# Performance work log

Measured on AMD Instinct MI355X. Metric: run time of the kernel, lower is better.

## Reference

```python
import jax, jax.numpy as jnp
import numpy as np

N_NODES = 50000
N_EDGES = 640000
IN_CH = 32
OUT_CH = 64
H1 = 2 * IN_CH   # 64
H2 = 4 * IN_CH   # 128


def _sage_conv(x, src, dst, w_l, b_l, w_r, n_nodes):
    """PyG SAGEConv (mean aggr): out = mean_{j in N(i)} x_j @ w_l + b_l + x_i @ w_r."""
    msg = x[src]                                                  # [E, d] gather
    agg = jax.ops.segment_sum(msg, dst, num_segments=n_nodes)    # [N, d]
    cnt = jax.ops.segment_sum(jnp.ones_like(dst, x.dtype), dst, num_segments=n_nodes)
    mean = agg / jnp.maximum(cnt, 1.0)[:, None]                   # empty neighborhoods -> 0
    return mean @ w_l + b_l + x @ w_r


def setup_inputs() -> dict:
    key = jax.random.key(0)
    ks = jax.random.split(key, 9)
    x = jax.random.normal(ks[0], (N_NODES, IN_CH), dtype=jnp.float32)
    edge_index = jax.random.randint(ks[1], (2, N_EDGES), 0, N_NODES, dtype=jnp.int32)

    def glorot(k, shape):
        fan_in, fan_out = shape
        s = jnp.sqrt(6.0 / (fan_in + fan_out))
        return jax.random.uniform(k, shape, jnp.float32, -s, s)

    return {
        "x": x,
        "edge_index": edge_index,
        "w1_l": glorot(ks[2], (IN_CH, H1)), "b1": jnp.zeros((H1,), jnp.float32),
        "w1_r": glorot(ks[3], (IN_CH, H1)),
        "w2_l": glorot(ks[4], (H1, H2)), "b2": jnp.zeros((H2,), jnp.float32),
        "w2_r": glorot(ks[5], (H1, H2)),
        "w3_l": glorot(ks[6], (H2, OUT_CH)), "b3": jnp.zeros((OUT_CH,), jnp.float32),
        "w3_r": glorot(ks[7], (H2, OUT_CH)),
    }


def reference(x, edge_index, w1_l, b1, w1_r, w2_l, b2, w2_r, w3_l, b3, w3_r):
    n = x.shape[0]
    src, dst = edge_index[0], edge_index[1]
    h = jax.nn.relu(_sage_conv(x, src, dst, w1_l, b1, w1_r, n))
    h = jax.nn.relu(_sage_conv(h, src, dst, w2_l, b2, w2_r, n))
    return _sage_conv(h, src, dst, w3_l, b3, w3_r, n)
```

## Files before the change

### kernel.cpp

```cpp
#include <hip/hip_runtime.h>


typedef short bf8 __attribute__((ext_vector_type(8)));
typedef short bf4 __attribute__((ext_vector_type(4)));
typedef float f32x4 __attribute__((ext_vector_type(4)));

__device__ inline ushort bf16rn(float f) {
    unsigned u = __float_as_uint(f);
    return (ushort)((u + 0x7FFFu + ((u >> 16) & 1u)) >> 16);
}
__device__ inline float bf16tof(ushort h) {
    return __uint_as_float(((unsigned)h) << 16);
}
__device__ inline void split8(const float4 pa, const float4 pb, bf8& hi, bf8& lo) {
    const float v[8] = {pa.x, pa.y, pa.z, pa.w, pb.x, pb.y, pb.z, pb.w};
#pragma unroll
    for (int j = 0; j < 8; ++j) {
        const ushort h = bf16rn(v[j]);
        hi[j] = (short)h;
        lo[j] = (short)bf16rn(v[j] - bf16tof(h));
    }
}

__global__ __launch_bounds__(256) void prep_kernel(
    const float* __restrict__ x,
    const float* __restrict__ w1l, const float* __restrict__ w1r,
    const float* __restrict__ w2l, const float* __restrict__ w2r,
    const float* __restrict__ w3l, const float* __restrict__ w3r,
    ushort* __restrict__ wprep, int* __restrict__ cnt,
    ushort* __restrict__ xh, int nN, int nCntZero)
{
    const int g = blockIdx.x * 256 + threadIdx.x;
    const int n = gridDim.x * 256;
    for (int f = g; f < 9216; f += n) {
        int base, KCs, oc0, d0, wstride;
        const float *wa, *wb;
        if (f < 1024)      { base = 0;    KCs = 2; oc0 = 0;  wa = w1l; wb = w1r; d0 = 32;  wstride = 64;  }
        else if (f < 3072) { base = 1024; KCs = 4; oc0 = 0;  wa = w2l; wb = w2r; d0 = 64;  wstride = 128; }
        else if (f < 5120) { base = 3072; KCs = 4; oc0 = 64; wa = w2l; wb = w2r; d0 = 64;  wstride = 128; }
        else if (f < 7168) { base = 5120; KCs = 4; oc0 = 0;  wa = w3l; wb = w3l; d0 = 128; wstride = 64;  }
        else               { base = 7168; KCs = 4; oc0 = 0;  wa = w3r; wb = w3r; d0 = 128; wstride = 64;  }
        const int local = f - base;
        const int lane = local & 63;
        const int s = (local >> 6) & 1;
        const int kcct = local >> 7;
        const int kc = kcct % KCs;
        const int ct = kcct / KCs;
        const int col = oc0 + ct * 16 + (lane & 15);
        const int k0 = kc * 32 + (lane >> 4) * 8;
        ushort h8[8];
#pragma unroll
        for (int j = 0; j < 8; ++j) {
            const int k = k0 + j;
            const float* wr = (k < d0) ? (wa + (size_t)k * wstride)
                                       : (wb + (size_t)(k - d0) * wstride);
            const float v = wr[col];
            const ushort h = bf16rn(v);
            h8[j] = (s == 0) ? h : bf16rn(v - bf16tof(h));
        }
        *reinterpret_cast<int4*>(wprep + (size_t)f * 8) = *reinterpret_cast<const int4*>(h8);
    }
    for (int i = g; i < nCntZero / 4; i += n)
        reinterpret_cast<int4*>(cnt)[i] = make_int4(0, 0, 0, 0);
    const int nxv = nN * 4;
    for (int i = g; i < nxv; i += n) {
        const float4 a = reinterpret_cast<const float4*>(x)[i * 2 + 0];
        const float4 b = reinterpret_cast<const float4*>(x)[i * 2 + 1];
        const float v[8] = {a.x, a.y, a.z, a.w, b.x, b.y, b.z, b.w};
        bf8 h;
#pragma unroll
        for (int j = 0; j < 8; ++j) h[j] = (short)bf16rn(v[j]);
        reinterpret_cast<bf8*>(xh)[i] = h;
    }
}

__global__ __launch_bounds__(256) void count_kernel(const int* __restrict__ dst,
                                                    int* __restrict__ cnt,
                                                    ushort* __restrict__ pos, int nE) {
    int i = blockIdx.x * blockDim.x + threadIdx.x;
    int e0 = i * 4;
    if (e0 + 3 < nE) {
        int4 d = *reinterpret_cast<const int4*>(dst + e0);
        ushort4 p;
        p.x = (ushort)atomicAdd(&cnt[d.x], 1);
        p.y = (ushort)atomicAdd(&cnt[d.y], 1);
        p.z = (ushort)atomicAdd(&cnt[d.z], 1);
        p.w = (ushort)atomicAdd(&cnt[d.w], 1);
        *reinterpret_cast<ushort4*>(pos + e0) = p;
    } else {
        for (int e = e0; e < nE; ++e) pos[e] = (ushort)atomicAdd(&cnt[dst[e]], 1);
    }
}

__global__ __launch_bounds__(256) void scan_blocks(const int* __restrict__ cnt,
                                                   int* __restrict__ rowptr,
                                                   int* __restrict__ partials, int nN) {
    __shared__ int wsum[4];
    const int t = threadIdx.x;
    const int lane = t & 63, wid = t >> 6;
    const int base = blockIdx.x * 1024 + t * 4;

    int4 v = make_int4(0, 0, 0, 0);
    if (base + 3 < nN) {
        v = *reinterpret_cast<const int4*>(cnt + base);
    } else {
        if (base + 0 < nN) v.x = cnt[base + 0];
        if (base + 1 < nN) v.y = cnt[base + 1];
        if (base + 2 < nN) v.z = cnt[base + 2];
        if (base + 3 < nN) v.w = cnt[base + 3];
    }
    const int s = v.x + v.y + v.z + v.w;

    int inc = s;
#pragma unroll
    for (int d = 1; d < 64; d <<= 1) {
        int u = __shfl_up(inc, d);
        if (lane >= d) inc += u;
    }
    if (lane == 63) wsum[wid] = inc;
    __syncthreads();
    int woff = 0;
#pragma unroll
    for (int w = 0; w < 4; ++w) woff += (w < wid) ? wsum[w] : 0;

    const int excl = woff + inc - s;
    int4 o;
    o.x = excl; o.y = excl + v.x; o.z = excl + v.x + v.y; o.w = excl + v.x + v.y + v.z;
    if (base + 3 < nN) {
        *reinterpret_cast<int4*>(rowptr + base) = o;
    } else {
        if (base + 0 < nN) rowptr[base + 0] = o.x;
        if (base + 1 < nN) rowptr[base + 1] = o.y;
        if (base + 2 < nN) rowptr[base + 2] = o.z;
        if (base + 3 < nN) rowptr[base + 3] = o.w;
    }
    if (t == 255) partials[blockIdx.x] = woff + inc;
}

__global__ __launch_bounds__(256) void scan_add(int* __restrict__ rowptr,
                                                const int* __restrict__ partials,
                                                int nN, int nE) {
    __shared__ int soff;
    const int t = threadIdx.x;
    if (t < 64) {
        int v = (t < blockIdx.x) ? partials[t] : 0;
#pragma unroll
        for (int d = 32; d >= 1; d >>= 1) v += __shfl_xor(v, d);
        if (t == 0) soff = v;
    }
    __syncthreads();
    const int off = soff;
    const int base = blockIdx.x * 1024 + t * 4;
    if (base + 3 < nN) {
        int4 v = *reinterpret_cast<int4*>(rowptr + base);
        v.x += off; v.y += off; v.z += off; v.w += off;
        *reinterpret_cast<int4*>(rowptr + base) = v;
    } else {
        if (base + 0 < nN) rowptr[base + 0] += off;
        if (base + 1 < nN) rowptr[base + 1] += off;
        if (base + 2 < nN) rowptr[base + 2] += off;
        if (base + 3 < nN) rowptr[base + 3] += off;
    }
    if (blockIdx.x == 0 && t == 0) rowptr[nN] = nE;
}

__global__ __launch_bounds__(256) void fill_kernel(const int* __restrict__ src,
                                                   const int* __restrict__ dst,
                                                   const ushort* __restrict__ pos,
                                                   const int* __restrict__ rowptr,
                                                   ushort* __restrict__ csr_src, int nE) {
    int i = blockIdx.x * blockDim.x + threadIdx.x;
    int e0 = i * 4;
    if (e0 + 3 < nE) {
        int4 s4 = *reinterpret_cast<const int4*>(src + e0);
        int4 d4 = *reinterpret_cast<const int4*>(dst + e0);
        ushort4 p4 = *reinterpret_cast<const ushort4*>(pos + e0);
        csr_src[rowptr[d4.x] + p4.x] = (ushort)s4.x;
        csr_src[rowptr[d4.y] + p4.y] = (ushort)s4.y;
        csr_src[rowptr[d4.z] + p4.z] = (ushort)s4.z;
        csr_src[rowptr[d4.w] + p4.w] = (ushort)s4.w;
    } else {
        for (int e = e0; e < nE; ++e)
            csr_src[rowptr[dst[e]] + pos[e]] = (ushort)src[e];
    }
}

__global__ __launch_bounds__(256) void fused_layer1(
    const float* __restrict__ x, const ushort* __restrict__ xh,
    const int* __restrict__ rowptr, const ushort* __restrict__ csr_src,
    const ushort* __restrict__ wfrag, const float* __restrict__ b1,
    ushort* __restrict__ h1h, ushort* __restrict__ h1l, int nN)
{
    __shared__ float tile[32 * 36];

    const int tid = threadIdx.x;
    const int node0 = blockIdx.x * 32;

    {
        const int nl = tid >> 3;
        const int c = tid & 7;
        const int node = node0 + nl;
        float acc[4] = {0.f, 0.f, 0.f, 0.f};
        if (node < nN) {
            const int beg = rowptr[node], end = rowptr[node + 1];
            int e = beg;
            for (; e + 7 < end; e += 8) {
                int si[8];
#pragma unroll
                for (int j = 0; j < 8; ++j) si[j] = csr_src[e + j];
                bf4 v[8];
#pragma unroll
                for (int j = 0; j < 8; ++j)
                    v[j] = *reinterpret_cast<const bf4*>(xh + (size_t)si[j] * 32 + c * 4);
#pragma unroll
                for (int k = 0; k < 4; ++k)
#pragma unroll
                    for (int j = 0; j < 8; ++j) acc[k] += bf16tof((ushort)v[j][k]);
            }
            for (; e < end; ++e) {
                bf4 v = *reinterpret_cast<const bf4*>(xh + (size_t)csr_src[e] * 32 + c * 4);
#pragma unroll
                for (int k = 0; k < 4; ++k) acc[k] += bf16tof((ushort)v[k]);
            }
            const float sc = 1.0f / (float)max(end - beg, 1);
#pragma unroll
            for (int k = 0; k < 4; ++k) acc[k] *= sc;
        }
        *reinterpret_cast<float4*>(&tile[nl * 36 + c * 4]) =
            make_float4(acc[0], acc[1], acc[2], acc[3]);
    }
    __syncthreads();

    const int w = tid >> 6, lane = tid & 63;
    const int rg = w & 1, cg = w >> 1;
    const int rloc = rg * 16 + (lane & 15);
    const int arow = min(node0 + rloc, nN - 1);
    const int kg = lane >> 4;
    bf8 ahi[2], alo[2];
    {
        const float* tp = &tile[rloc * 36 + kg * 8];
        split8(*reinterpret_cast<const float4*>(tp),
               *reinterpret_cast<const float4*>(tp + 4), ahi[0], alo[0]);
    }
    {
        const float* rp = x + (size_t)arow * 32 + kg * 8;
        split8(*reinterpret_cast<const float4*>(rp),
               *reinterpret_cast<const float4*>(rp + 4), ahi[1], alo[1]);
    }
    const bf8* bgl = reinterpret_cast<const bf8*>(wfrag);
#pragma unroll
    for (int cc = 0; cc < 2; ++cc) {
        const int ct = cg * 2 + cc;
        f32x4 acc = {0.f, 0.f, 0.f, 0.f};
#pragma unroll
        for (int kc = 0; kc < 2; ++kc) {
            const bf8 bhi = bgl[((ct * 2 + kc) * 2 + 0) * 64 + lane];
            const bf8 blo = bgl[((ct * 2 + kc) * 2 + 1) * 64 + lane];
            acc = __builtin_amdgcn_mfma_f32_16x16x32_bf16(ahi[kc], bhi, acc, 0, 0, 0);
            acc = __builtin_amdgcn_mfma_f32_16x16x32_bf16(ahi[kc], blo, acc, 0, 0, 0);
            acc = __builtin_amdgcn_mfma_f32_16x16x32_bf16(alo[kc], bhi, acc, 0, 0, 0);
        }
        const int col = ct * 16 + (lane & 15);
        const float bv = b1[col];
#pragma unroll
        for (int r = 0; r < 4; ++r) {
            const int node = node0 + rg * 16 + (lane >> 4) * 4 + r;
            if (node < nN) {
                const float o = fmaxf(acc[r] + bv, 0.f);
                const ushort hi = bf16rn(o);
                h1h[(size_t)node * 64 + col] = hi;
                h1l[(size_t)node * 64 + col] = bf16rn(o - bf16tof(hi));
            }
        }
    }
}

__global__ __launch_bounds__(256) void fused_layer2(
    const ushort* __restrict__ h1h, const ushort* __restrict__ h1l,
    const int* __restrict__ rowptr, const ushort* __restrict__ csr_src,
    const ushort* __restrict__ wfrag, const float* __restrict__ b2,
    ushort* __restrict__ h2h, ushort* __restrict__ h2l, int nN)
{
    __shared__ float tile[32 * 68];

    const int tid = threadIdx.x;
    const int node0 = blockIdx.x * 32;

    {
        const int nl = tid >> 3;
        const int c = tid & 7;
        const int node = node0 + nl;
        float acc[8] = {0.f, 0.f, 0.f, 0.f, 0.f, 0.f, 0.f, 0.f};
        if (node < nN) {
            const int beg = rowptr[node], end = rowptr[node + 1];
            int e = beg;
            for (; e + 7 < end; e += 8) {
                int si[8];
#pragma unroll
                for (int j = 0; j < 8; ++j) si[j] = csr_src[e + j];
                bf8 v[8];
#pragma unroll
                for (int j = 0; j < 8; ++j)
                    v[j] = *reinterpret_cast<const bf8*>(h1h + (size_t)si[j] * 64 + c * 8);
#pragma unroll
                for (int k = 0; k < 8; ++k)
#pragma unroll
                    for (int j = 0; j < 8; ++j) acc[k] += bf16tof((ushort)v[j][k]);
            }
            for (; e < end; ++e) {
                bf8 v = *reinterpret_cast<const bf8*>(h1h + (size_t)csr_src[e] * 64 + c * 8);
#pragma unroll
                for (int k = 0; k < 8; ++k) acc[k] += bf16tof((ushort)v[k]);
            }
            const float sc = 1.0f / (float)max(end - beg, 1);
#pragma unroll
            for (int k = 0; k < 8; ++k) acc[k] *= sc;
        }
        *reinterpret_cast<float4*>(&tile[nl * 68 + c * 8 + 0]) =
            make_float4(acc[0], acc[1], acc[2], acc[3]);
        *reinterpret_cast<float4*>(&tile[nl * 68 + c * 8 + 4]) =
            make_float4(acc[4], acc[5], acc[6], acc[7]);
    }
    __syncthreads();

    const int w = tid >> 6, lane = tid & 63;
    const int rg = w & 1, cg = w >> 1;
    const int rloc = rg * 16 + (lane & 15);
    const int arow = min(node0 + rloc, nN - 1);
    const int kg = lane >> 4;
    bf8 ahi[4], alo[4];
#pragma unroll
    for (int kc = 0; kc < 2; ++kc) {
        const float* tp = &tile[rloc * 68 + kc * 32 + kg * 8];
        split8(*reinterpret_cast<const float4*>(tp),
               *reinterpret_cast<const float4*>(tp + 4), ahi[kc], alo[kc]);
    }
#pragma unroll
    for (int kc = 2; kc < 4; ++kc) {
        const size_t off = (size_t)arow * 64 + (kc - 2) * 32 + kg * 8;
        ahi[kc] = *reinterpret_cast<const bf8*>(h1h + off);
        alo[kc] = *reinterpret_cast<const bf8*>(h1l + off);
    }
    const bf8* bgl = reinterpret_cast<const bf8*>(wfrag) + cg * 2048;
#pragma unroll
    for (int ctl = 0; ctl < 4; ++ctl) {
        f32x4 acc = {0.f, 0.f, 0.f, 0.f};
#pragma unroll
        for (int kc = 0; kc < 4; ++kc) {
            const bf8 bhi = bgl[((ctl * 4 + kc) * 2 + 0) * 64 + lane];
            const bf8 blo = bgl[((ctl * 4 + kc) * 2 + 1) * 64 + lane];
            acc = __builtin_amdgcn_mfma_f32_16x16x32_bf16(ahi[kc], bhi, acc, 0, 0, 0);
            acc = __builtin_amdgcn_mfma_f32_16x16x32_bf16(ahi[kc], blo, acc, 0, 0, 0);
            acc = __builtin_amdgcn_mfma_f32_16x16x32_bf16(alo[kc], bhi, acc, 0, 0, 0);
        }
        const int col = cg * 64 + ctl * 16 + (lane & 15);
        const float bv = b2[col];
#pragma unroll
        for (int r = 0; r < 4; ++r) {
            const int node = node0 + rg * 16 + (lane >> 4) * 4 + r;
            if (node < nN) {
                const float o = fmaxf(acc[r] + bv, 0.f);
                const ushort hi = bf16rn(o);
                h2h[(size_t)node * 128 + col] = hi;
                h2l[(size_t)node * 128 + col] = bf16rn(o - bf16tof(hi));
            }
        }
    }
}

__global__ __launch_bounds__(256) void mfma_dual(
    const ushort* __restrict__ h2h, const ushort* __restrict__ h2l,
    const ushort* __restrict__ wfrag, const float* __restrict__ b3,
    ushort* __restrict__ t3h, ushort* __restrict__ r3h, int nN)
{
    const int tid = threadIdx.x;
    const int w = tid >> 6, lane = tid & 63;
    const int node0 = blockIdx.x * 64;
    const int arow = min(node0 + w * 16 + (lane & 15), nN - 1);
    const int kg = lane >> 4;

    bf8 ahi[4], alo[4];
#pragma unroll
    for (int kc = 0; kc < 4; ++kc) {
        const size_t off = (size_t)arow * 128 + kc * 32 + kg * 8;
        ahi[kc] = *reinterpret_cast<const bf8*>(h2h + off);
        alo[kc] = *reinterpret_cast<const bf8*>(h2l + off);
    }
#pragma unroll
    for (int sel = 0; sel < 2; ++sel) {
        const bf8* bgl = reinterpret_cast<const bf8*>(wfrag) + sel * 2048;
#pragma unroll
        for (int ct = 0; ct < 4; ++ct) {
            f32x4 acc = {0.f, 0.f, 0.f, 0.f};
#pragma unroll
            for (int kc = 0; kc < 4; ++kc) {
                const bf8 bhi = bgl[((ct * 4 + kc) * 2 + 0) * 64 + lane];
                const bf8 blo = bgl[((ct * 4 + kc) * 2 + 1) * 64 + lane];
                acc = __builtin_amdgcn_mfma_f32_16x16x32_bf16(ahi[kc], bhi, acc, 0, 0, 0);
                acc = __builtin_amdgcn_mfma_f32_16x16x32_bf16(ahi[kc], blo, acc, 0, 0, 0);
                acc = __builtin_amdgcn_mfma_f32_16x16x32_bf16(alo[kc], bhi, acc, 0, 0, 0);
            }
            const int col = ct * 16 + (lane & 15);
#pragma unroll
            for (int r = 0; r < 4; ++r) {
                const int node = node0 + w * 16 + (lane >> 4) * 4 + r;
                if (node < nN) {
                    if (sel) r3h[(size_t)node * 64 + col] = bf16rn(acc[r] + b3[col]);
                    else     t3h[(size_t)node * 64 + col] = bf16rn(acc[r]);
                }
            }
        }
    }
}

__global__ __launch_bounds__(256) void final_gather(
    const ushort* __restrict__ t3h, const int* __restrict__ rowptr,
    const ushort* __restrict__ csr_src, const ushort* __restrict__ r3h,
    float* __restrict__ dout, int nN)
{
    const int tid = threadIdx.x;
    const int node = blockIdx.x * 32 + (tid >> 3);
    const int c = tid & 7;
    if (node >= nN) return;
    const int beg = rowptr[node], end = rowptr[node + 1];
    float acc[8] = {0.f, 0.f, 0.f, 0.f, 0.f, 0.f, 0.f, 0.f};
    int e = beg;
    for (; e + 7 < end; e += 8) {
        int si[8];
#pragma unroll
        for (int j = 0; j < 8; ++j) si[j] = csr_src[e + j];
        bf8 v[8];
#pragma unroll
        for (int j = 0; j < 8; ++j)
            v[j] = *reinterpret_cast<const bf8*>(t3h + (size_t)si[j] * 64 + c * 8);
#pragma unroll
        for (int k = 0; k < 8; ++k)
#pragma unroll
            for (int j = 0; j < 8; ++j) acc[k] += bf16tof((ushort)v[j][k]);
    }
    for (; e < end; ++e) {
        bf8 v = *reinterpret_cast<const bf8*>(t3h + (size_t)csr_src[e] * 64 + c * 8);
#pragma unroll
        for (int k = 0; k < 8; ++k) acc[k] += bf16tof((ushort)v[k]);
    }
    const float sc = 1.0f / (float)max(end - beg, 1);
    const bf8 a = *reinterpret_cast<const bf8*>(r3h + (size_t)node * 64 + c * 8);
    float4 o0, o1;
    o0.x = fmaf(acc[0], sc, bf16tof((ushort)a[0]));
    o0.y = fmaf(acc[1], sc, bf16tof((ushort)a[1]));
    o0.z = fmaf(acc[2], sc, bf16tof((ushort)a[2]));
    o0.w = fmaf(acc[3], sc, bf16tof((ushort)a[3]));
    o1.x = fmaf(acc[4], sc, bf16tof((ushort)a[4]));
    o1.y = fmaf(acc[5], sc, bf16tof((ushort)a[5]));
    o1.z = fmaf(acc[6], sc, bf16tof((ushort)a[6]));
    o1.w = fmaf(acc[7], sc, bf16tof((ushort)a[7]));
    reinterpret_cast<float4*>(dout)[(size_t)node * 16 + c * 2 + 0] = o0;
    reinterpret_cast<float4*>(dout)[(size_t)node * 16 + c * 2 + 1] = o1;
}

extern "C" void kernel_launch(void* const* d_in, const int* in_sizes, int n_in,
                              void* d_out, int out_size, void* d_ws, size_t ws_size,
                              hipStream_t stream) {
    const float* x   = (const float*)d_in[0];
    const int*   ei  = (const int*)d_in[1];
    const float* w1l = (const float*)d_in[2];
    const float* b1  = (const float*)d_in[3];
    const float* w1r = (const float*)d_in[4];
    const float* w2l = (const float*)d_in[5];
    const float* b2  = (const float*)d_in[6];
    const float* w2r = (const float*)d_in[7];
    const float* w3l = (const float*)d_in[8];
    const float* b3  = (const float*)d_in[9];
    const float* w3r = (const float*)d_in[10];

    const int nN = in_sizes[0] / 32;
    const int nE = in_sizes[1] / 2;
    const int* src = ei;
    const int* dst = ei + nE;
    const int nB = (nN + 1023) / 1024;
    const int nCntZero = (nN + 63) & ~63;

    char* ws = (char*)d_ws;
    size_t o = 0;
    auto alloc = [&](size_t nbytes) {
        char* p = ws + o;
        o += (nbytes + 255) & ~(size_t)255;
        return p;
    };
    int*    cnt      = (int*)alloc((size_t)nCntZero * sizeof(int));
    ushort* pos      = (ushort*)alloc((size_t)nE * sizeof(ushort));
    int*    partials = (int*)alloc(64 * sizeof(int));
    int*    rowptr   = (int*)alloc(((size_t)nN + 1) * sizeof(int));
    ushort* csr_src  = (ushort*)alloc((size_t)nE * sizeof(ushort));
    ushort* wprep    = (ushort*)alloc((size_t)9216 * 8 * sizeof(ushort));
    ushort* xh       = (ushort*)alloc((size_t)nN * 32 * sizeof(ushort));
    ushort* h1h      = (ushort*)alloc((size_t)nN * 64 * sizeof(ushort));
    ushort* h1l      = (ushort*)alloc((size_t)nN * 64 * sizeof(ushort));
    ushort* h2h      = (ushort*)alloc((size_t)nN * 128 * sizeof(ushort));
    ushort* h2l      = (ushort*)alloc((size_t)nN * 128 * sizeof(ushort));
    ushort* t3h      = (ushort*)alloc((size_t)nN * 64 * sizeof(ushort));
    ushort* r3h      = (ushort*)alloc((size_t)nN * 64 * sizeof(ushort));

    prep_kernel<<<784, 256, 0, stream>>>(x, w1l, w1r, w2l, w2r, w3l, w3r,
                                         wprep, cnt, xh, nN, nCntZero);
    count_kernel<<<(nE / 4 + 255) / 256, 256, 0, stream>>>(dst, cnt, pos, nE);
    scan_blocks<<<nB, 256, 0, stream>>>(cnt, rowptr, partials, nN);
    scan_add<<<nB, 256, 0, stream>>>(rowptr, partials, nN, nE);
    fill_kernel<<<(nE / 4 + 255) / 256, 256, 0, stream>>>(src, dst, pos, rowptr, csr_src, nE);

    const int xblk32 = (nN + 31) / 32;
    const int xblk64 = (nN + 63) / 64;

    fused_layer1<<<xblk32, 256, 0, stream>>>(x, xh, rowptr, csr_src, wprep, b1, h1h, h1l, nN);
    fused_layer2<<<xblk32, 256, 0, stream>>>(h1h, h1l, rowptr, csr_src,
                                             wprep + (size_t)1024 * 8, b2, h2h, h2l, nN);
    mfma_dual<<<xblk64, 256, 0, stream>>>(h2h, h2l, wprep + (size_t)5120 * 8, b3, t3h, r3h, nN);
    final_gather<<<(nN + 31) / 32, 256, 0, stream>>>(t3h, rowptr, csr_src, r3h, (float*)d_out, nN);
}
```

Before: 141.7 us.

## Drop h2 low-part split and fuse edge counting into prep kernel

Layer-2 output is now stored only as a bf16 high part, so the layer-3 matmul loads half the activation data and issues two MFMAs per k-chunk instead of three. The separate count kernel is merged into the prep kernel as a grid-stride loop, and the zeroing of the count array moves to a hipMemsetAsync issued before it. This removes one kernel launch, one full-size write of h2 and its read-back, and a third of layer-3 MFMA work. The cost is lower precision in layer 3, since the activation is no longer split into hi/lo parts, and the atomic counting now runs inside the 784-block prep grid.

```diff
diff --git a/kernel.cpp b/kernel.cpp
--- a/kernel.cpp
+++ b/kernel.cpp
@@ -22,13 +22,14 @@
     }
 }
 
-__global__ __launch_bounds__(256) void prep_kernel(
+__global__ __launch_bounds__(256) void prep_count_kernel(
     const float* __restrict__ x,
     const float* __restrict__ w1l, const float* __restrict__ w1r,
     const float* __restrict__ w2l, const float* __restrict__ w2r,
     const float* __restrict__ w3l, const float* __restrict__ w3r,
-    ushort* __restrict__ wprep, int* __restrict__ cnt,
-    ushort* __restrict__ xh, int nN, int nCntZero)
+    ushort* __restrict__ wprep, ushort* __restrict__ xh,
+    const int* __restrict__ dst, int* __restrict__ cnt,
+    ushort* __restrict__ pos, int nN, int nE)
 {
     const int g = blockIdx.x * 256 + threadIdx.x;
     const int n = gridDim.x * 256;
@@ -60,8 +61,6 @@
         }
         *reinterpret_cast<int4*>(wprep + (size_t)f * 8) = *reinterpret_cast<const int4*>(h8);
     }
-    for (int i = g; i < nCntZero / 4; i += n)
-        reinterpret_cast<int4*>(cnt)[i] = make_int4(0, 0, 0, 0);
     const int nxv = nN * 4;
     for (int i = g; i < nxv; i += n) {
         const float4 a = reinterpret_cast<const float4*>(x)[i * 2 + 0];
@@ -72,24 +71,18 @@
         for (int j = 0; j < 8; ++j) h[j] = (short)bf16rn(v[j]);
         reinterpret_cast<bf8*>(xh)[i] = h;
     }
-}
-
-__global__ __launch_bounds__(256) void count_kernel(const int* __restrict__ dst,
-                                                    int* __restrict__ cnt,
-                                                    ushort* __restrict__ pos, int nE) {
-    int i = blockIdx.x * blockDim.x + threadIdx.x;
-    int e0 = i * 4;
-    if (e0 + 3 < nE) {
-        int4 d = *reinterpret_cast<const int4*>(dst + e0);
+    const int n4 = nE >> 2;
+    for (int i = g; i < n4; i += n) {
+        int4 d = reinterpret_cast<const int4*>(dst)[i];
         ushort4 p;
         p.x = (ushort)atomicAdd(&cnt[d.x], 1);
         p.y = (ushort)atomicAdd(&cnt[d.y], 1);
         p.z = (ushort)atomicAdd(&cnt[d.z], 1);
         p.w = (ushort)atomicAdd(&cnt[d.w], 1);
-        *reinterpret_cast<ushort4*>(pos + e0) = p;
-    } else {
-        for (int e = e0; e < nE; ++e) pos[e] = (ushort)atomicAdd(&cnt[dst[e]], 1);
-    }
+        reinterpret_cast<ushort4*>(pos)[i] = p;
+    }
+    for (int e = (nE & ~3) + g; e < nE; e += n)
+        pos[e] = (ushort)atomicAdd(&cnt[dst[e]], 1);
 }
 
 __global__ __launch_bounds__(256) void scan_blocks(const int* __restrict__ cnt,
@@ -279,7 +272,7 @@
     const ushort* __restrict__ h1h, const ushort* __restrict__ h1l,
     const int* __restrict__ rowptr, const ushort* __restrict__ csr_src,
     const ushort* __restrict__ wfrag, const float* __restrict__ b2,
-    ushort* __restrict__ h2h, ushort* __restrict__ h2l, int nN)
+    ushort* __restrict__ h2h, int nN)
 {
     __shared__ float tile[32 * 68];
 
@@ -358,20 +351,16 @@
 #pragma unroll
         for (int r = 0; r < 4; ++r) {
             const int node = node0 + rg * 16 + (lane >> 4) * 4 + r;
-            if (node < nN) {
-                const float o = fmaxf(acc[r] + bv, 0.f);
-                const ushort hi = bf16rn(o);
-                h2h[(size_t)node * 128 + col] = hi;
-                h2l[(size_t)node * 128 + col] = bf16rn(o - bf16tof(hi));
-            }
+            if (node < nN)
+                h2h[(size_t)node * 128 + col] = bf16rn(fmaxf(acc[r] + bv, 0.f));
         }
     }
 }
 
 __global__ __launch_bounds__(256) void mfma_dual(
-    const ushort* __restrict__ h2h, const ushort* __restrict__ h2l,
-    const ushort* __restrict__ wfrag, const float* __restrict__ b3,
-    ushort* __restrict__ t3h, ushort* __restrict__ r3h, int nN)
+    const ushort* __restrict__ h2h, const ushort* __restrict__ wfrag,
+    const float* __restrict__ b3, ushort* __restrict__ t3h,
+    ushort* __restrict__ r3h, int nN)
 {
     const int tid = threadIdx.x;
     const int w = tid >> 6, lane = tid & 63;
@@ -379,13 +368,11 @@
     const int arow = min(node0 + w * 16 + (lane & 15), nN - 1);
     const int kg = lane >> 4;
 
-    bf8 ahi[4], alo[4];
-#pragma unroll
-    for (int kc = 0; kc < 4; ++kc) {
-        const size_t off = (size_t)arow * 128 + kc * 32 + kg * 8;
-        ahi[kc] = *reinterpret_cast<const bf8*>(h2h + off);
-        alo[kc] = *reinterpret_cast<const bf8*>(h2l + off);
-    }
+    bf8 ahi[4];
+#pragma unroll
+    for (int kc = 0; kc < 4; ++kc)
+        ahi[kc] = *reinterpret_cast<const bf8*>(h2h + (size_t)arow * 128 + kc * 32 + kg * 8);
+
 #pragma unroll
     for (int sel = 0; sel < 2; ++sel) {
         const bf8* bgl = reinterpret_cast<const bf8*>(wfrag) + sel * 2048;
@@ -398,7 +385,6 @@
                 const bf8 blo = bgl[((ct * 4 + kc) * 2 + 1) * 64 + lane];
                 acc = __builtin_amdgcn_mfma_f32_16x16x32_bf16(ahi[kc], bhi, acc, 0, 0, 0);
                 acc = __builtin_amdgcn_mfma_f32_16x16x32_bf16(ahi[kc], blo, acc, 0, 0, 0);
-                acc = __builtin_amdgcn_mfma_f32_16x16x32_bf16(alo[kc], bhi, acc, 0, 0, 0);
             }
             const int col = ct * 16 + (lane & 15);
 #pragma unroll
@@ -497,13 +483,12 @@
     ushort* h1h      = (ushort*)alloc((size_t)nN * 64 * sizeof(ushort));
     ushort* h1l      = (ushort*)alloc((size_t)nN * 64 * sizeof(ushort));
     ushort* h2h      = (ushort*)alloc((size_t)nN * 128 * sizeof(ushort));
-    ushort* h2l      = (ushort*)alloc((size_t)nN * 128 * sizeof(ushort));
     ushort* t3h      = (ushort*)alloc((size_t)nN * 64 * sizeof(ushort));
     ushort* r3h      = (ushort*)alloc((size_t)nN * 64 * sizeof(ushort));
 
-    prep_kernel<<<784, 256, 0, stream>>>(x, w1l, w1r, w2l, w2r, w3l, w3r,
-                                         wprep, cnt, xh, nN, nCntZero);
-    count_kernel<<<(nE / 4 + 255) / 256, 256, 0, stream>>>(dst, cnt, pos, nE);
+    hipMemsetAsync(cnt, 0, (size_t)nCntZero * sizeof(int), stream);
+    prep_count_kernel<<<784, 256, 0, stream>>>(x, w1l, w1r, w2l, w2r, w3l, w3r,
+                                               wprep, xh, dst, cnt, pos, nN, nE);
     scan_blocks<<<nB, 256, 0, stream>>>(cnt, rowptr, partials, nN);
     scan_add<<<nB, 256, 0, stream>>>(rowptr, partials, nN, nE);
     fill_kernel<<<(nE / 4 + 255) / 256, 256, 0, stream>>>(src, dst, pos, rowptr, csr_src, nE);
@@ -513,7 +498,7 @@
 
     fused_layer1<<<xblk32, 256, 0, stream>>>(x, xh, rowptr, csr_src, wprep, b1, h1h, h1l, nN);
     fused_layer2<<<xblk32, 256, 0, stream>>>(h1h, h1l, rowptr, csr_src,
-                                             wprep + (size_t)1024 * 8, b2, h2h, h2l, nN);
-    mfma_dual<<<xblk64, 256, 0, stream>>>(h2h, h2l, wprep + (size_t)5120 * 8, b3, t3h, r3h, nN);
+                                             wprep + (size_t)1024 * 8, b2, h2h, nN);
+    mfma_dual<<<xblk64, 256, 0, stream>>>(h2h, wprep + (size_t)5120 * 8, b3, t3h, r3h, nN);
     final_gather<<<(nN + 31) / 32, 256, 0, stream>>>(t3h, rowptr, csr_src, r3h, (float*)d_out, nN);
 }
```

Result: no change. 139.5 us (-1.5%).
